# Performance work log

Measured on AMD Instinct MI355X. Metric: run time of the kernel, lower is better.

Reference implementation:

```python
import jax, jax.numpy as jnp
import numpy as np

B, C = 8, 256
GRID = 128          # H = W = grid_size
N = GRID * GRID     # 16384 tokens
WS = 8              # swin window size
NH = 8              # num heads
DH = C // NH        # head dim = 32
HID = int(C * 4.0)  # mlp hidden = 1024
EPS = 1e-5


def _ln(x, g, b):
    m = jnp.mean(x, axis=-1, keepdims=True)
    v = jnp.mean(jnp.square(x - m), axis=-1, keepdims=True)
    return (x - m) * jax.lax.rsqrt(v + EPS) * g + b


def setup_inputs() -> dict:
    key = jax.random.key(0)
    ks = jax.random.split(key, 6)
    s = 0.02
    return {
        "x": jax.random.normal(ks[0], (B, N, C), jnp.float32),
        "ln1_g": jnp.ones((C,), jnp.float32), "ln1_b": jnp.zeros((C,), jnp.float32),
        "in_w": jax.random.normal(ks[1], (3 * C, C), jnp.float32) * s,
        "in_b": jnp.zeros((3 * C,), jnp.float32),
        "out_w": jax.random.normal(ks[2], (C, C), jnp.float32) * s,
        "out_b": jnp.zeros((C,), jnp.float32),
        "ln2_g": jnp.ones((C,), jnp.float32), "ln2_b": jnp.zeros((C,), jnp.float32),
        "w1": jax.random.normal(ks[3], (HID, C), jnp.float32) * s,
        "b1": jnp.zeros((HID,), jnp.float32),
        "w2": jax.random.normal(ks[4], (C, HID), jnp.float32) * s,
        "b2": jnp.zeros((C,), jnp.float32),
    }


def reference(x, ln1_g, ln1_b, in_w, in_b, out_w, out_b, ln2_g, ln2_b, w1, b1, w2, b2):
    shortcut = x
    xn = _ln(x, ln1_g, ln1_b)
    # window partition: [B,N,C] -> [B,H,W,C] -> [B*nW, WS*WS, C]
    xw = (xn.reshape(B, GRID // WS, WS, GRID // WS, WS, C)
            .transpose(0, 1, 3, 2, 4, 5)
            .reshape(-1, WS * WS, C))
    # torch nn.MultiheadAttention: fused in-proj, scale 1/sqrt(head_dim)
    qkv = xw @ in_w.T + in_b                      # [nW, T, 3C]
    q, k, v = jnp.split(qkv, 3, axis=-1)
    def heads(t):
        return t.reshape(t.shape[0], t.shape[1], NH, DH).transpose(0, 2, 1, 3)
    q, k, v = heads(q), heads(k), heads(v)        # [nW, NH, T, DH]
    scores = jnp.einsum('whtd,whsd->whts', q, k) * (1.0 / np.sqrt(DH))
    att = jax.nn.softmax(scores, axis=-1)
    o = jnp.einsum('whts,whsd->whtd', att, v)     # [nW, NH, T, DH]
    o = o.transpose(0, 2, 1, 3).reshape(-1, WS * WS, C)
    o = o @ out_w.T + out_b
    # window reverse: [B*nW, WS, WS, C] -> [B, N, C]
    x_attn = (o.reshape(B, GRID // WS, GRID // WS, WS, WS, C)
                .transpose(0, 1, 3, 2, 4, 5)
                .reshape(B, N, C))
    x = shortcut + x_attn
    h = _ln(x, ln2_g, ln2_b)
    h = jax.nn.gelu(h @ w1.T + b1, approximate=False)  # torch nn.GELU = exact erf
    return x + h @ w2.T + b2
```

## Files before the change

kernel.cpp:

```cpp
#include <hip/hip_runtime.h>
#include <hip/hip_bf16.h>
#include <cstdint>

#define DEVINL __device__ __forceinline__

using bf16 = __hip_bfloat16;
typedef __bf16 bf16x8 __attribute__((ext_vector_type(8)));
typedef float f32x4 __attribute__((ext_vector_type(4)));
typedef unsigned short u16x8 __attribute__((ext_vector_type(8)));

static constexpr int MTOK = 131072;

DEVINL void async_ld16(const void* g, void* l) {
  __builtin_amdgcn_global_load_lds(
      (__attribute__((address_space(1))) void*)(g),
      (__attribute__((address_space(3))) void*)(l), 16, 0, 0);
}

DEVINL unsigned short bfbits(float v) {
  bf16 h = __float2bfloat16(v);
  return *reinterpret_cast<unsigned short*>(&h);
}

DEVINL long pkaddr(long m, int k, int KP) {
  const long tile = m >> 7;
  const int row = (int)(m & 127);
  const int panel = k >> 6;
  const int c8 = ((k & 63) >> 3) ^ (row & 7);
  return ((tile * KP + panel) * 1024 + row * 8 + c8) * 8 + (k & 7);
}

__global__ __launch_bounds__(256) void cvt_w2(
    const float* __restrict__ ow, const float* __restrict__ w1,
    const float* __restrict__ w2, bf16* __restrict__ out) {
  int i = blockIdx.x * 256 + threadIdx.x;
  float v; long base; int n, k, KP;
  if (i < 65536)        { v = ow[i]; base = 0;      n = i >> 8;  k = i & 255;  KP = 4; }
  else if (i < 327680)  { int j = i - 65536;  v = w1[j]; base = 65536;  n = j >> 8;  k = j & 255;  KP = 4; }
  else                  { int j = i - 327680; v = w2[j]; base = 327680; n = j >> 10; k = j & 1023; KP = 16; }
  out[base + pkaddr(n, k, KP)] = __float2bfloat16(v);
}

template <bool REMAP>
__global__ __launch_bounds__(256) void ln_kern(
    const float* __restrict__ x, const float* __restrict__ gw,
    const float* __restrict__ bw, bf16* __restrict__ out) {
  const int lane = threadIdx.x & 63;
  const int wv = threadIdx.x >> 6;
  const long tok = (long)blockIdx.x * 4 + wv;
  const float4 v = *(const float4*)(x + tok * 256 + lane * 4);
  float s = v.x + v.y + v.z + v.w;
#pragma unroll
  for (int off = 32; off > 0; off >>= 1) s += __shfl_xor(s, off);
  const float mean = s * (1.0f / 256.0f);
  const float dx = v.x - mean, dy = v.y - mean, dz = v.z - mean, dw = v.w - mean;
  float q = dx * dx + dy * dy + dz * dz + dw * dw;
#pragma unroll
  for (int off = 32; off > 0; off >>= 1) q += __shfl_xor(q, off);
  const float inv = rsqrtf(q * (1.0f / 256.0f) + 1e-5f);
  long m;
  if (REMAP) {
    const int b = (int)(tok >> 14);
    const int n = (int)(tok & 16383);
    const int row = n >> 7, col = n & 127;
    const int w = b * 256 + (row >> 3) * 16 + (col >> 3);
    const int t = (row & 7) * 8 + (col & 7);
    m = (long)w * 64 + t;
  } else {
    m = tok;
  }
  const float4 g = *(const float4*)(gw + lane * 4);
  const float4 bb = *(const float4*)(bw + lane * 4);
  ushort4 o;
  o.x = bfbits(dx * inv * g.x + bb.x);
  o.y = bfbits(dy * inv * g.y + bb.y);
  o.z = bfbits(dz * inv * g.z + bb.z);
  o.w = bfbits(dw * inv * g.w + bb.w);
  *(ushort4*)((unsigned short*)out + pkaddr(m, lane * 4, 4)) = o;
}

enum { EPI_QKV = 0, EPI_OUTPROJ = 1, EPI_GELU = 2, EPI_RESID = 3 };

template <int KP, int EPI, bool BF32>
__global__ __launch_bounds__(256) void gemm_db(
    const bf16* __restrict__ A, const void* __restrict__ Bw,
    const float* __restrict__ bias,
    bf16* __restrict__ oQ, bf16* __restrict__ oK, bf16* __restrict__ oV,
    const float* __restrict__ resid, float* __restrict__ of32,
    bf16* __restrict__ obf) {
  __shared__ __align__(16) unsigned short As[2][128 * 64];
  __shared__ __align__(16) unsigned short Bs[2][128 * 64];
  const int tid = threadIdx.x;
  const int lane = tid & 63, wv = tid >> 6;
  const int quad = lane >> 4, l16 = lane & 15;
  const int wm = wv >> 1, wn = wv & 1;
  const int gx = gridDim.x;
  const int nwg = gx * gridDim.y;
  const int orig = blockIdx.x + gx * blockIdx.y;
  const int wg = (orig & 7) * (nwg >> 3) + (orig >> 3);
  const int ntile = wg % gx;
  const long mtile = wg / gx;
  const long m0 = mtile * 128;
  const int n0 = ntile * 128;

  const bf16* Bp = (const bf16*)Bw;
  const float* Bf = (const float*)Bw;
  float4 br[4][2];

  auto stageA = [&](int i, int buf) {
    const bf16* Apan = A + (mtile * KP + i) * 8192;
#pragma unroll
    for (int p = 0; p < 4; ++p) {
      const int f = p * 256 + tid;
      async_ld16(Apan + f * 8, (char*)&As[buf][0] + f * 16);
    }
  };
  auto stageB = [&](int i, int buf) {
    const bf16* Bpan = Bp + ((long)ntile * KP + i) * 8192;
#pragma unroll
    for (int p = 0; p < 4; ++p) {
      const int f = p * 256 + tid;
      async_ld16(Bpan + f * 8, (char*)&Bs[buf][0] + f * 16);
    }
  };
  auto issueB = [&](int i) {
#pragma unroll
    for (int p = 0; p < 4; ++p) {
      const int f = p * 256 + tid, row = f >> 3;
      const int chunk = (f & 7) ^ (row & 7);
      const float* src = Bf + (long)(n0 + row) * 256 + i * 64 + chunk * 8;
      br[p][0] = *(const float4*)(src);
      br[p][1] = *(const float4*)(src + 4);
    }
  };
  auto writeB = [&](int buf) {
#pragma unroll
    for (int p = 0; p < 4; ++p) {
      const int f = p * 256 + tid;
      u16x8 o;
      o[0] = bfbits(br[p][0].x); o[1] = bfbits(br[p][0].y);
      o[2] = bfbits(br[p][0].z); o[3] = bfbits(br[p][0].w);
      o[4] = bfbits(br[p][1].x); o[5] = bfbits(br[p][1].y);
      o[6] = bfbits(br[p][1].z); o[7] = bfbits(br[p][1].w);
      *(u16x8*)((char*)&Bs[buf][0] + f * 16) = o;
    }
  };

  const f32x4 fz = {0.f, 0.f, 0.f, 0.f};
  f32x4 acc[4][4];
#pragma unroll
  for (int a = 0; a < 4; ++a) {
#pragma unroll
    for (int b = 0; b < 4; ++b) acc[a][b] = fz;
  }

  if constexpr (BF32) { issueB(0); stageA(0, 0); }
  else                { stageA(0, 0); stageB(0, 0); }

#pragma unroll 1
  for (int i = 0; i < KP; ++i) {
    if constexpr (BF32) writeB(i & 1);
    __syncthreads();
    if (i + 1 < KP) {
      if constexpr (BF32) { issueB(i + 1); stageA(i + 1, (i + 1) & 1); }
      else                { stageA(i + 1, (i + 1) & 1); stageB(i + 1, (i + 1) & 1); }
    }
    const unsigned short* Asb = &As[i & 1][0];
    const unsigned short* Bsb = &Bs[i & 1][0];
#pragma unroll
    for (int kk = 0; kk < 2; ++kk) {
      bf16x8 af[4], bfr[4];
#pragma unroll
      for (int mt = 0; mt < 4; ++mt) {
        const int row = wm * 64 + mt * 16 + l16;
        const int c8 = (kk * 4 + quad) ^ (row & 7);
        af[mt] = *(const bf16x8*)(Asb + row * 64 + c8 * 8);
      }
#pragma unroll
      for (int nt = 0; nt < 4; ++nt) {
        const int row = wn * 64 + nt * 16 + l16;
        const int c8 = (kk * 4 + quad) ^ (row & 7);
        bfr[nt] = *(const bf16x8*)(Bsb + row * 64 + c8 * 8);
      }
#pragma unroll
      for (int mt = 0; mt < 4; ++mt) {
#pragma unroll
        for (int nt = 0; nt < 4; ++nt) {
          acc[mt][nt] = __builtin_amdgcn_mfma_f32_16x16x32_bf16(
              af[mt], bfr[nt], acc[mt][nt], 0, 0, 0);
        }
      }
    }
  }

#pragma unroll
  for (int mt = 0; mt < 4; ++mt) {
#pragma unroll
    for (int nt = 0; nt < 4; ++nt) {
      const long mb = m0 + wm * 64 + mt * 16 + quad * 4;
      const int j = n0 + wn * 64 + nt * 16 + l16;
      const float bj = bias[j];
#pragma unroll
      for (int r = 0; r < 4; ++r) {
        const long m = mb + r;
        const float v = acc[mt][nt][r] + bj;
        if constexpr (EPI == EPI_QKV) {
          const int w = (int)(m >> 6), t = (int)(m & 63);
          const int region = j >> 8, hh = (j >> 5) & 7, d = j & 31;
          const long hb = (long)w * 8 + hh;
          if (region == 0)      oQ[(hb * 64 + t) * 32 + d] = __float2bfloat16(v);
          else if (region == 1) oK[(hb * 64 + t) * 32 + d] = __float2bfloat16(v);
          else                  oV[(hb * 32 + d) * 64 + t] = __float2bfloat16(v);
        } else if constexpr (EPI == EPI_OUTPROJ) {
          const int w = (int)(m >> 6), t = (int)(m & 63);
          const int b = w >> 8, wi = w & 255;
          const int row = (wi >> 4) * 8 + (t >> 3);
          const int col = (wi & 15) * 8 + (t & 7);
          const long addr = ((long)b * 16384 + row * 128 + col) * 256 + j;
          of32[addr] = v + resid[addr];
        } else if constexpr (EPI == EPI_GELU) {
          const float g = 0.5f * v * (1.0f + erff(v * 0.70710678118654752f));
          obf[pkaddr(m, j, 16)] = __float2bfloat16(g);
        } else {
          const long addr = m * 256 + j;
          of32[addr] += v;
        }
      }
    }
  }
}

__global__ __launch_bounds__(256) void attn_kern(
    const bf16* __restrict__ Qb, const bf16* __restrict__ Kb,
    const bf16* __restrict__ Vtb, bf16* __restrict__ O) {
  __shared__ __align__(16) unsigned short P[4][64 * 72];
  const int lane = threadIdx.x & 63;
  const int wv = threadIdx.x >> 6;
  const int quad = lane >> 4, l16 = lane & 15;
  const long w = blockIdx.x;
  unsigned short* Pw = &P[wv][0];
  const float SC = 0.17677669529663689f;
  const f32x4 fz = {0.f, 0.f, 0.f, 0.f};

#pragma unroll 1
  for (int hi = 0; hi < 2; ++hi) {
    const int h = wv * 2 + hi;
    const bf16* qp = Qb + ((w * 8 + h) * 64) * 32;
    const bf16* kp = Kb + ((w * 8 + h) * 64) * 32;
    const bf16* vt = Vtb + ((w * 8 + h) * 32) * 64;

    bf16x8 qf[4], kf[4];
#pragma unroll
    for (int mt = 0; mt < 4; ++mt)
      qf[mt] = *(const bf16x8*)(qp + (mt * 16 + l16) * 32 + quad * 8);
#pragma unroll
    for (int nt = 0; nt < 4; ++nt)
      kf[nt] = *(const bf16x8*)(kp + (nt * 16 + l16) * 32 + quad * 8);

    f32x4 s[4][4];
#pragma unroll
    for (int a = 0; a < 4; ++a) {
#pragma unroll
      for (int b = 0; b < 4; ++b) s[a][b] = fz;
    }
#pragma unroll
    for (int mt = 0; mt < 4; ++mt) {
#pragma unroll
      for (int nt = 0; nt < 4; ++nt) {
        s[mt][nt] = __builtin_amdgcn_mfma_f32_16x16x32_bf16(qf[mt], kf[nt],
                                                            s[mt][nt], 0, 0, 0);
      }
    }

#pragma unroll
    for (int mt = 0; mt < 4; ++mt) {
#pragma unroll
      for (int r = 0; r < 4; ++r) {
        float a0 = s[mt][0][r] * SC, a1 = s[mt][1][r] * SC;
        float a2 = s[mt][2][r] * SC, a3 = s[mt][3][r] * SC;
        float mx = fmaxf(fmaxf(a0, a1), fmaxf(a2, a3));
#pragma unroll
        for (int off = 8; off > 0; off >>= 1) mx = fmaxf(mx, __shfl_xor(mx, off));
        a0 = __expf(a0 - mx); a1 = __expf(a1 - mx);
        a2 = __expf(a2 - mx); a3 = __expf(a3 - mx);
        float sm = a0 + a1 + a2 + a3;
#pragma unroll
        for (int off = 8; off > 0; off >>= 1) sm += __shfl_xor(sm, off);
        const float iv = 1.0f / sm;
        const int rp = (mt * 16 + quad * 4 + r) * 72;
        Pw[rp + l16]      = bfbits(a0 * iv);
        Pw[rp + 16 + l16] = bfbits(a1 * iv);
        Pw[rp + 32 + l16] = bfbits(a2 * iv);
        Pw[rp + 48 + l16] = bfbits(a3 * iv);
      }
    }

    bf16x8 vf[2][2];
#pragma unroll
    for (int kt = 0; kt < 2; ++kt) {
#pragma unroll
      for (int dt = 0; dt < 2; ++dt)
        vf[kt][dt] = *(const bf16x8*)(vt + (dt * 16 + l16) * 64 + kt * 32 + quad * 8);
    }
    f32x4 oa[4][2];
#pragma unroll
    for (int a = 0; a < 4; ++a) { oa[a][0] = fz; oa[a][1] = fz; }
#pragma unroll
    for (int mt = 0; mt < 4; ++mt) {
      const unsigned short* pr = Pw + (mt * 16 + l16) * 72 + quad * 8;
      const bf16x8 p0 = *(const bf16x8*)(pr);
      const bf16x8 p1 = *(const bf16x8*)(pr + 32);
#pragma unroll
      for (int dt = 0; dt < 2; ++dt) {
        oa[mt][dt] = __builtin_amdgcn_mfma_f32_16x16x32_bf16(p0, vf[0][dt], oa[mt][dt], 0, 0, 0);
        oa[mt][dt] = __builtin_amdgcn_mfma_f32_16x16x32_bf16(p1, vf[1][dt], oa[mt][dt], 0, 0, 0);
      }
    }

#pragma unroll
    for (int mt = 0; mt < 4; ++mt) {
#pragma unroll
      for (int dt = 0; dt < 2; ++dt) {
#pragma unroll
        for (int r = 0; r < 4; ++r) {
          const long m = w * 64 + mt * 16 + quad * 4 + r;
          const int k = h * 32 + dt * 16 + l16;
          O[pkaddr(m, k, 4)] = __float2bfloat16(oa[mt][dt][r]);
        }
      }
    }
  }
}

extern "C" void kernel_launch(void* const* d_in, const int* in_sizes, int n_in,
                              void* d_out, int out_size, void* d_ws, size_t ws_size,
                              hipStream_t stream) {
  const float* x     = (const float*)d_in[0];
  const float* ln1g  = (const float*)d_in[1];
  const float* ln1b  = (const float*)d_in[2];
  const float* in_w  = (const float*)d_in[3];
  const float* in_b  = (const float*)d_in[4];
  const float* out_w = (const float*)d_in[5];
  const float* out_b = (const float*)d_in[6];
  const float* ln2g  = (const float*)d_in[7];
  const float* ln2b  = (const float*)d_in[8];
  const float* w1    = (const float*)d_in[9];
  const float* b1    = (const float*)d_in[10];
  const float* w2    = (const float*)d_in[11];
  const float* b2    = (const float*)d_in[12];
  float* out = (float*)d_out;

  char* ws = (char*)d_ws;
  const size_t MB = 1ull << 20;
  bf16* XW   = (bf16*)ws;
  bf16* Qb   = (bf16*)(ws + 64 * MB);
  bf16* Kb   = (bf16*)(ws + 128 * MB);
  bf16* Vtb  = (bf16*)(ws + 192 * MB);
  bf16* WB   = (bf16*)(ws + 64 * MB);
  bf16* Wo   = WB;
  bf16* W1c  = WB + 65536;
  bf16* W2c  = WB + 327680;
  bf16* H1   = (bf16*)(ws + 66 * MB);
  bf16* Obuf = XW;
  bf16* Hbuf = XW;

  ln_kern<true><<<MTOK / 4, 256, 0, stream>>>(x, ln1g, ln1b, XW);
  gemm_db<4, EPI_QKV, true><<<dim3(6, MTOK / 128), 256, 0, stream>>>(
      XW, in_w, in_b, Qb, Kb, Vtb, nullptr, nullptr, nullptr);
  attn_kern<<<2048, 256, 0, stream>>>(Qb, Kb, Vtb, Obuf);
  cvt_w2<<<2304, 256, 0, stream>>>(out_w, w1, w2, WB);
  gemm_db<4, EPI_OUTPROJ, false><<<dim3(2, MTOK / 128), 256, 0, stream>>>(
      Obuf, Wo, out_b, nullptr, nullptr, nullptr, x, out, nullptr);
  ln_kern<false><<<MTOK / 4, 256, 0, stream>>>(out, ln2g, ln2b, Hbuf);
  for (int c = 0; c < 2; ++c) {
    gemm_db<4, EPI_GELU, false><<<dim3(8, 512), 256, 0, stream>>>(
        Hbuf + (long)c * 16777216, W1c, b1,
        nullptr, nullptr, nullptr, nullptr, nullptr, H1);
    gemm_db<16, EPI_RESID, false><<<dim3(2, 512), 256, 0, stream>>>(
        H1, W2c, b2, nullptr, nullptr, nullptr, nullptr,
        out + (long)c * 16777216, nullptr);
  }
}
```

Before: 926.1 us.

## Stage GEMM and attention epilogues through LDS for coalesced 16-byte stores

The QKV, GELU and attention-output epilogues previously wrote scattered 2-byte bf16 values straight to global memory. They now write the tile into shared memory, reusing the GEMM operand buffers or a new per-wave buffer in attention, then copy it out with 16-byte vector stores in the destination's packed or head-major layout. The V region is transposed in LDS so its token-contiguous output also gets wide stores. This adds barriers, LDS traffic and, in attention, more shared memory per block, which may reduce occupancy.

```diff
diff --git a/kernel.cpp b/kernel.cpp
--- a/kernel.cpp
+++ b/kernel.cpp
@@ -88,8 +88,7 @@
     bf16* __restrict__ oQ, bf16* __restrict__ oK, bf16* __restrict__ oV,
     const float* __restrict__ resid, float* __restrict__ of32,
     bf16* __restrict__ obf) {
-  __shared__ __align__(16) unsigned short As[2][128 * 64];
-  __shared__ __align__(16) unsigned short Bs[2][128 * 64];
+  __shared__ __align__(16) unsigned short smem[32768];
   const int tid = threadIdx.x;
   const int lane = tid & 63, wv = tid >> 6;
   const int quad = lane >> 4, l16 = lane & 15;
@@ -112,7 +111,7 @@
 #pragma unroll
     for (int p = 0; p < 4; ++p) {
       const int f = p * 256 + tid;
-      async_ld16(Apan + f * 8, (char*)&As[buf][0] + f * 16);
+      async_ld16(Apan + f * 8, (char*)smem + buf * 16384 + f * 16);
     }
   };
   auto stageB = [&](int i, int buf) {
@@ -120,7 +119,7 @@
 #pragma unroll
     for (int p = 0; p < 4; ++p) {
       const int f = p * 256 + tid;
-      async_ld16(Bpan + f * 8, (char*)&Bs[buf][0] + f * 16);
+      async_ld16(Bpan + f * 8, (char*)smem + 32768 + buf * 16384 + f * 16);
     }
   };
   auto issueB = [&](int i) {
@@ -142,7 +141,7 @@
       o[2] = bfbits(br[p][0].z); o[3] = bfbits(br[p][0].w);
       o[4] = bfbits(br[p][1].x); o[5] = bfbits(br[p][1].y);
       o[6] = bfbits(br[p][1].z); o[7] = bfbits(br[p][1].w);
-      *(u16x8*)((char*)&Bs[buf][0] + f * 16) = o;
+      *(u16x8*)((char*)smem + 32768 + buf * 16384 + f * 16) = o;
     }
   };
 
@@ -165,8 +164,8 @@
       if constexpr (BF32) { issueB(i + 1); stageA(i + 1, (i + 1) & 1); }
       else                { stageA(i + 1, (i + 1) & 1); stageB(i + 1, (i + 1) & 1); }
     }
-    const unsigned short* Asb = &As[i & 1][0];
-    const unsigned short* Bsb = &Bs[i & 1][0];
+    const unsigned short* Asb = smem + (i & 1) * 8192;
+    const unsigned short* Bsb = smem + 16384 + (i & 1) * 8192;
 #pragma unroll
     for (int kk = 0; kk < 2; ++kk) {
       bf16x8 af[4], bfr[4];
@@ -193,37 +192,105 @@
     }
   }
 
-#pragma unroll
-  for (int mt = 0; mt < 4; ++mt) {
-#pragma unroll
-    for (int nt = 0; nt < 4; ++nt) {
-      const long mb = m0 + wm * 64 + mt * 16 + quad * 4;
-      const int j = n0 + wn * 64 + nt * 16 + l16;
-      const float bj = bias[j];
-#pragma unroll
-      for (int r = 0; r < 4; ++r) {
-        const long m = mb + r;
-        const float v = acc[mt][nt][r] + bj;
-        if constexpr (EPI == EPI_QKV) {
-          const int w = (int)(m >> 6), t = (int)(m & 63);
-          const int region = j >> 8, hh = (j >> 5) & 7, d = j & 31;
-          const long hb = (long)w * 8 + hh;
-          if (region == 0)      oQ[(hb * 64 + t) * 32 + d] = __float2bfloat16(v);
-          else if (region == 1) oK[(hb * 64 + t) * 32 + d] = __float2bfloat16(v);
-          else                  oV[(hb * 32 + d) * 64 + t] = __float2bfloat16(v);
-        } else if constexpr (EPI == EPI_OUTPROJ) {
-          const int w = (int)(m >> 6), t = (int)(m & 63);
-          const int b = w >> 8, wi = w & 255;
-          const int row = (wi >> 4) * 8 + (t >> 3);
-          const int col = (wi & 15) * 8 + (t & 7);
-          const long addr = ((long)b * 16384 + row * 128 + col) * 256 + j;
-          of32[addr] = v + resid[addr];
-        } else if constexpr (EPI == EPI_GELU) {
-          const float g = 0.5f * v * (1.0f + erff(v * 0.70710678118654752f));
-          obf[pkaddr(m, j, 16)] = __float2bfloat16(g);
-        } else {
-          const long addr = m * 256 + j;
-          of32[addr] += v;
+  if constexpr (EPI == EPI_QKV || EPI == EPI_GELU) {
+    const int region = (EPI == EPI_QKV) ? (n0 >> 8) : 0;
+    float bj4[4];
+#pragma unroll
+    for (int nt = 0; nt < 4; ++nt) bj4[nt] = bias[n0 + wn * 64 + nt * 16 + l16];
+    __syncthreads();
+    if (EPI == EPI_GELU || region < 2) {
+#pragma unroll
+      for (int mt = 0; mt < 4; ++mt) {
+#pragma unroll
+        for (int nt = 0; nt < 4; ++nt) {
+          const int j_l = wn * 64 + nt * 16 + l16;
+#pragma unroll
+          for (int r = 0; r < 4; ++r) {
+            const int m_l = wm * 64 + mt * 16 + quad * 4 + r;
+            float v = acc[mt][nt][r] + bj4[nt];
+            if constexpr (EPI == EPI_GELU)
+              v = 0.5f * v * (1.0f + erff(v * 0.70710678118654752f));
+            smem[m_l * 136 + j_l] = bfbits(v);
+          }
+        }
+      }
+    } else {
+#pragma unroll
+      for (int mt = 0; mt < 4; ++mt) {
+#pragma unroll
+        for (int nt = 0; nt < 4; ++nt) {
+          const int j_l = wn * 64 + nt * 16 + l16;
+          const int m_b = wm * 64 + mt * 16 + quad * 4;
+          ushort4 pk;
+          pk.x = bfbits(acc[mt][nt][0] + bj4[nt]);
+          pk.y = bfbits(acc[mt][nt][1] + bj4[nt]);
+          pk.z = bfbits(acc[mt][nt][2] + bj4[nt]);
+          pk.w = bfbits(acc[mt][nt][3] + bj4[nt]);
+          *(ushort4*)(smem + j_l * 136 + m_b) = pk;
+        }
+      }
+    }
+    __syncthreads();
+    if constexpr (EPI == EPI_QKV) {
+      bf16* dst0 = (region == 0) ? oQ : ((region == 1) ? oK : oV);
+      const int hbase = (n0 >> 5) & 7;
+      const long w0 = m0 >> 6;
+      if (region < 2) {
+#pragma unroll
+        for (int p = 0; p < 8; ++p) {
+          const int u = p * 256 + tid;
+          const int c = u >> 8, rr = u & 255;
+          const int t = rr >> 2, d0 = (rr & 3) * 8;
+          const unsigned short* src = smem + ((c >> 2) * 64 + t) * 136 + (c & 3) * 32 + d0;
+          const long hb = (w0 + (c >> 2)) * 8 + hbase + (c & 3);
+          *(u16x8*)((unsigned short*)dst0 + (hb * 64 + t) * 32 + d0) = *(const u16x8*)src;
+        }
+      } else {
+#pragma unroll
+        for (int p = 0; p < 8; ++p) {
+          const int u = p * 256 + tid;
+          const int c = u >> 8, rr = u & 255;
+          const int d = rr >> 3, t0 = (rr & 7) * 8;
+          const unsigned short* src = smem + ((c & 3) * 32 + d) * 136 + (c >> 2) * 64 + t0;
+          const long hb = (w0 + (c >> 2)) * 8 + hbase + (c & 3);
+          *(u16x8*)((unsigned short*)dst0 + (hb * 32 + d) * 64 + t0) = *(const u16x8*)src;
+        }
+      }
+    } else {
+      const int p0 = n0 >> 6;
+#pragma unroll
+      for (int p = 0; p < 8; ++p) {
+        const int u = p * 256 + tid;
+        const int p_l = u >> 10, g = u & 1023;
+        const int row = g >> 3, c8 = g & 7;
+        const unsigned short* src = smem + row * 136 + p_l * 64 + ((c8 ^ (row & 7)) * 8);
+        unsigned short* dst = (unsigned short*)obf + ((mtile * 16 + p0 + p_l) * 1024 + g) * 8;
+        *(u16x8*)dst = *(const u16x8*)src;
+      }
+    }
+  } else {
+#pragma unroll
+    for (int mt = 0; mt < 4; ++mt) {
+#pragma unroll
+      for (int nt = 0; nt < 4; ++nt) {
+        const long mb = m0 + wm * 64 + mt * 16 + quad * 4;
+        const int j = n0 + wn * 64 + nt * 16 + l16;
+        const float bj = bias[j];
+#pragma unroll
+        for (int r = 0; r < 4; ++r) {
+          const long m = mb + r;
+          const float v = acc[mt][nt][r] + bj;
+          if constexpr (EPI == EPI_OUTPROJ) {
+            const int w = (int)(m >> 6), t = (int)(m & 63);
+            const int b = w >> 8, wi = w & 255;
+            const int row = (wi >> 4) * 8 + (t >> 3);
+            const int col = (wi & 15) * 8 + (t & 7);
+            const long addr = ((long)b * 16384 + row * 128 + col) * 256 + j;
+            of32[addr] = v + resid[addr];
+          } else {
+            const long addr = m * 256 + j;
+            of32[addr] += v;
+          }
         }
       }
     }
@@ -234,11 +301,13 @@
     const bf16* __restrict__ Qb, const bf16* __restrict__ Kb,
     const bf16* __restrict__ Vtb, bf16* __restrict__ O) {
   __shared__ __align__(16) unsigned short P[4][64 * 72];
+  __shared__ __align__(16) unsigned short Cw[4][64 * 72];
   const int lane = threadIdx.x & 63;
   const int wv = threadIdx.x >> 6;
   const int quad = lane >> 4, l16 = lane & 15;
   const long w = blockIdx.x;
   unsigned short* Pw = &P[wv][0];
+  unsigned short* Cww = &Cw[wv][0];
   const float SC = 0.17677669529663689f;
   const f32x4 fz = {0.f, 0.f, 0.f, 0.f};
 
@@ -323,12 +392,25 @@
       for (int dt = 0; dt < 2; ++dt) {
 #pragma unroll
         for (int r = 0; r < 4; ++r) {
-          const long m = w * 64 + mt * 16 + quad * 4 + r;
-          const int k = h * 32 + dt * 16 + l16;
-          O[pkaddr(m, k, 4)] = __float2bfloat16(oa[mt][dt][r]);
-        }
-      }
-    }
+          const int m_l = mt * 16 + quad * 4 + r;
+          const int j_l = hi * 32 + dt * 16 + l16;
+          Cww[m_l * 72 + j_l] = bfbits(oa[mt][dt][r]);
+        }
+      }
+    }
+  }
+
+  __syncthreads();
+  const long tile = w >> 1;
+  const int half = (int)(w & 1);
+#pragma unroll
+  for (int p = 0; p < 8; ++p) {
+    const int u = p * 64 + lane;
+    const int row = u >> 3, c8 = u & 7;
+    const unsigned short* src = Cww + row * 72 + ((c8 ^ (row & 7)) * 8);
+    unsigned short* dst = (unsigned short*)O +
+        ((tile * 4 + wv) * 1024 + (half * 64 + row) * 8 + c8) * 8;
+    *(u16x8*)dst = *(const u16x8*)src;
   }
 }
 
```

Result: faster. 812.0 us (-12.3%).
